# Optimization experiments

Measured on AMD Instinct MI355X. Metric: run time of the kernel, lower is better.

The kernel has to match this reference:

```python
import jax, jax.numpy as jnp
import numpy as np

DIM = 1024
HEADS = 16
HEAD_DIM = DIM // HEADS
SCALE = HEAD_DIM ** -0.5


def setup_inputs() -> dict:
    key = jax.random.key(0)
    ks = jax.random.split(key, 6)
    B, N, C = 2, 2048, DIM
    q = jax.random.normal(ks[0], (B, N, C), dtype=jnp.float32)
    k = jax.random.normal(ks[1], (B, N, C), dtype=jnp.float32)
    v = jax.random.normal(ks[2], (B, N, C), dtype=jnp.float32)
    # torch nn.Linear weights: out = x @ W.T (+ b); qkv has no bias (qkv_bias=False)
    W_qkv = jax.random.normal(ks[3], (3 * C, 3 * C), dtype=jnp.float32) * (3 * C) ** -0.5
    W_proj = jax.random.normal(ks[4], (C, C), dtype=jnp.float32) * C ** -0.5
    b_proj = jax.random.normal(ks[5], (C,), dtype=jnp.float32) * 0.02
    return {"q": q, "k": k, "v": v, "W_qkv": W_qkv, "W_proj": W_proj, "b_proj": b_proj}


def reference(q, k, v, W_qkv, W_proj, b_proj):
    B, N, C = q.shape
    # fused QKV projection on concatenated [q,k,v] -> [B,N,3C]
    qkv = jnp.concatenate([q, k, v], axis=-1) @ W_qkv.T
    qkv = qkv.reshape(B, N, 3, HEADS, HEAD_DIM).transpose(2, 0, 3, 1, 4)  # [3,B,H,N,hd]
    qh, kh, vh = qkv[0], qkv[1], qkv[2]
    attn = jnp.einsum('bhqd,bhkd->bhqk', qh, kh) * SCALE
    attn = jax.nn.softmax(attn, axis=-1)  # attn_drop is identity (p=0)
    x = jnp.einsum('bhqk,bhkd->bhqd', attn, vh)  # [B,H,N,hd]
    x = x.transpose(0, 2, 1, 3).reshape(B, N, C)
    x = x @ W_proj.T + b_proj  # proj_drop is identity (p=0)
    return x
```

## Files before the change

kernel.cpp:

```cpp
#include <hip/hip_runtime.h>
#include <hip/hip_bf16.h>
#include <stdint.h>

#define HEADS 16
#define HD 64
#define SEQ 2048
#define BATCH 2
#define CDIM 1024
#define MROWS (BATCH*SEQ)
#define K3C (3*CDIM)
#define QSCALE 0.1803368801111244f

typedef __bf16 bf16x8 __attribute__((ext_vector_type(8)));
typedef float  f32x4  __attribute__((ext_vector_type(4)));

__device__ __forceinline__ unsigned short f2bf(float f) {
    __hip_bfloat16 h = __float2bfloat16(f);
    return __builtin_bit_cast(unsigned short, h);
}
__device__ __forceinline__ unsigned int pack2bf(float a, float b) {
    return (unsigned int)f2bf(a) | ((unsigned int)f2bf(b) << 16);
}
__device__ __forceinline__ bf16x8 frag(uint4 u) { return __builtin_bit_cast(bf16x8, u); }

__device__ __forceinline__ void async16(const unsigned short* g, unsigned short* lds) {
    __builtin_amdgcn_global_load_lds(
        (const __attribute__((address_space(1))) unsigned int*)g,
        (__attribute__((address_space(3))) unsigned int*)lds, 16, 0, 0);
}

__global__ void cast_all(const float* __restrict__ q, const float* __restrict__ k,
                         const float* __restrict__ v, const float* __restrict__ Wq,
                         const float* __restrict__ Wp,
                         unsigned short* __restrict__ A, unsigned short* __restrict__ Wqb,
                         unsigned short* __restrict__ Wpb)
{
    const int bid = blockIdx.x;
    const int t = threadIdx.x;
    if (bid < MROWS) {
        const float* srcs[3] = {q, k, v};
        #pragma unroll
        for (int i = 0; i < 3; ++i) {
            float4 f = *(const float4*)(srcs[i] + (size_t)bid*CDIM + t*4);
            ushort4 s;
            s.x = f2bf(f.x); s.y = f2bf(f.y); s.z = f2bf(f.z); s.w = f2bf(f.w);
            *(ushort4*)(A + (size_t)bid*K3C + i*CDIM + t*4) = s;
        }
    } else if (bid < MROWS + 9216) {
        int idx = (bid - MROWS)*256 + t;
        float4 f = ((const float4*)Wq)[idx];
        ushort4 s;
        s.x = f2bf(f.x); s.y = f2bf(f.y); s.z = f2bf(f.z); s.w = f2bf(f.w);
        ((ushort4*)Wqb)[idx] = s;
    } else {
        int idx = (bid - MROWS - 9216)*256 + t;
        float4 f = ((const float4*)Wp)[idx];
        ushort4 s;
        s.x = f2bf(f.x); s.y = f2bf(f.y); s.z = f2bf(f.z); s.w = f2bf(f.w);
        ((ushort4*)Wpb)[idx] = s;
    }
}

template<int EPI>
__global__ __launch_bounds__(256, 2)
void gemm_bt(const unsigned short* __restrict__ A, const unsigned short* __restrict__ B,
             int M, int N, int K,
             unsigned short* __restrict__ qh, unsigned short* __restrict__ kh,
             unsigned short* __restrict__ vt,
             const float* __restrict__ bias, float* __restrict__ out)
{
    __shared__ __attribute__((aligned(16))) unsigned short As[128*32];
    __shared__ __attribute__((aligned(16))) unsigned short Bs[128*32];
    const int tid  = threadIdx.x;
    const int wave = tid >> 6;
    const int lane = tid & 63;
    const int l15  = lane & 15;
    const int quad = lane >> 4;
    const int wm = (wave >> 1) * 64;
    const int wn = (wave & 1) * 64;
    const int m0 = blockIdx.x * 128;
    const int n0 = blockIdx.y * 128;

    f32x4 acc[4][4] = {};

    const int srow = tid >> 2;
    const int sc8  = (tid & 3) * 8;

    for (int k0 = 0; k0 < K; k0 += 32) {
        #pragma unroll
        for (int t = 0; t < 2; ++t) {
            int row = t*64 + srow;
            const unsigned short* ga = A + (size_t)(m0 + row)*K + k0 + sc8;
            const unsigned short* gb = B + (size_t)(n0 + row)*K + k0 + sc8;
            async16(ga, &As[(t*256 + wave*64)*8]);
            async16(gb, &Bs[(t*256 + wave*64)*8]);
        }
        __syncthreads();
        uint4 af[4], bfv[4];
        #pragma unroll
        for (int i = 0; i < 4; ++i) {
            af[i]  = *(const uint4*)&As[(wm + i*16 + l15)*32 + quad*8];
            bfv[i] = *(const uint4*)&Bs[(wn + i*16 + l15)*32 + quad*8];
        }
        #pragma unroll
        for (int mi = 0; mi < 4; ++mi)
            #pragma unroll
            for (int ni = 0; ni < 4; ++ni)
                acc[mi][ni] = __builtin_amdgcn_mfma_f32_16x16x32_bf16(
                    frag(af[mi]), frag(bfv[ni]), acc[mi][ni], 0, 0, 0);
        __syncthreads();
    }

    if constexpr (EPI == 0) {
        #pragma unroll
        for (int mi = 0; mi < 4; ++mi) {
            int row0 = m0 + wm + mi*16 + quad*4;
            int b  = row0 >> 11;
            int nq = row0 & 2047;
            #pragma unroll
            for (int ni = 0; ni < 4; ++ni) {
                int col   = n0 + wn + ni*16 + l15;
                int which = col >> 10;
                int h     = (col >> 6) & 15;
                int d     = col & 63;
                int bh    = b*HEADS + h;
                if (which == 2) {
                    ushort4 pv;
                    pv.x = f2bf(acc[mi][ni][0]);
                    pv.y = f2bf(acc[mi][ni][1]);
                    pv.z = f2bf(acc[mi][ni][2]);
                    pv.w = f2bf(acc[mi][ni][3]);
                    *(ushort4*)&vt[((size_t)bh*HD + d)*SEQ + nq] = pv;
                } else {
                    unsigned short* dst = (which == 0) ? qh : kh;
                    float sc = (which == 0) ? QSCALE : 1.0f;
                    #pragma unroll
                    for (int r = 0; r < 4; ++r)
                        dst[((size_t)bh*SEQ + nq + r)*HD + d] = f2bf(acc[mi][ni][r] * sc);
                }
            }
        }
    } else {
        #pragma unroll
        for (int mi = 0; mi < 4; ++mi) {
            int row0 = m0 + wm + mi*16 + quad*4;
            #pragma unroll
            for (int ni = 0; ni < 4; ++ni) {
                int col  = n0 + wn + ni*16 + l15;
                float bv = bias[col];
                #pragma unroll
                for (int r = 0; r < 4; ++r)
                    out[(size_t)(row0 + r)*N + col] = acc[mi][ni][r] + bv;
            }
        }
    }
}

__global__ __launch_bounds__(256, 2)
void attention(const unsigned short* __restrict__ qh, const unsigned short* __restrict__ kh,
               const unsigned short* __restrict__ vt, unsigned short* __restrict__ xb)
{
    const int qt = blockIdx.x;
    const int h  = blockIdx.y;
    const int b  = blockIdx.z;
    const int bh = b*HEADS + h;
    const int tid  = threadIdx.x;
    const int wave = tid >> 6;
    const int lane = tid & 63;
    const int l15  = lane & 15;
    const int quad = lane >> 4;

    __shared__ __attribute__((aligned(16))) unsigned short Ks[2][64*64];
    __shared__ __attribute__((aligned(16))) unsigned short Vs[2][64*64];
    __shared__ __attribute__((aligned(16))) unsigned short Ps[4][2*16*72];

    const unsigned short* Qp = qh + ((size_t)bh*SEQ + qt*128 + wave*32)*HD;
    const unsigned short* Kp = kh + (size_t)bh*SEQ*HD;
    const unsigned short* Vp = vt + (size_t)bh*HD*SEQ;

    auto stage = [&](int kt, int bufI) {
        #pragma unroll
        for (int t = 0; t < 2; ++t) {
            int c  = t*256 + wave*64 + lane;
            int r  = c >> 3;
            int cc = (c & 7) ^ (r & 7);
            async16(Kp + (size_t)(kt*64 + r)*HD + cc*8,
                    &Ks[bufI][(t*256 + wave*64)*8]);
            async16(Vp + (size_t)r*SEQ + kt*64 + cc*8,
                    &Vs[bufI][(t*256 + wave*64)*8]);
        }
    };

    stage(0, 0);

    uint4 qf[2][2];
    #pragma unroll
    for (int g = 0; g < 2; ++g) {
        qf[g][0] = *(const uint4*)(Qp + (size_t)(g*16 + l15)*HD + quad*8);
        qf[g][1] = *(const uint4*)(Qp + (size_t)(g*16 + l15)*HD + 32 + quad*8);
    }

    f32x4 o[2][4] = {};
    float m_s[2] = {-INFINITY, -INFINITY};
    float l_s[2] = {0.f, 0.f};

    unsigned short* Pw = Ps[wave];
    const int x7 = l15 & 7;

    for (int kt = 0; kt < SEQ/64; ++kt) {
        stage((kt + 1) & 31, (kt + 1) & 1);
        asm volatile("s_waitcnt vmcnt(4)" ::: "memory");
        asm volatile("s_barrier" ::: "memory");

        const unsigned short* Kb = Ks[kt & 1];
        const unsigned short* Vb = Vs[kt & 1];

        f32x4 s[2][4];
        #pragma unroll
        for (int st = 0; st < 4; ++st) {
            int rb = st*16 + l15;
            uint4 kf0 = *(const uint4*)&Kb[(rb*8 + (quad ^ x7))*8];
            uint4 kf1 = *(const uint4*)&Kb[(rb*8 + ((4 + quad) ^ x7))*8];
            #pragma unroll
            for (int g = 0; g < 2; ++g) {
                f32x4 z = {};
                z = __builtin_amdgcn_mfma_f32_16x16x32_bf16(frag(kf0), frag(qf[g][0]), z, 0, 0, 0);
                z = __builtin_amdgcn_mfma_f32_16x16x32_bf16(frag(kf1), frag(qf[g][1]), z, 0, 0, 0);
                s[g][st] = z;
            }
        }

        #pragma unroll
        for (int g = 0; g < 2; ++g) {
            float mloc = s[g][0][0];
            #pragma unroll
            for (int st = 0; st < 4; ++st)
                #pragma unroll
                for (int r = 0; r < 4; ++r)
                    mloc = fmaxf(mloc, s[g][st][r]);
            mloc = fmaxf(mloc, __shfl_xor(mloc, 16));
            mloc = fmaxf(mloc, __shfl_xor(mloc, 32));

            float mn = fmaxf(m_s[g], mloc);
            float al = __builtin_amdgcn_exp2f(m_s[g] - mn);
            m_s[g] = mn;

            float rs = 0.f;
            float p[4][4];
            #pragma unroll
            for (int st = 0; st < 4; ++st)
                #pragma unroll
                for (int r = 0; r < 4; ++r) {
                    p[st][r] = __builtin_amdgcn_exp2f(s[g][st][r] - mn);
                    rs += p[st][r];
                }
            rs += __shfl_xor(rs, 16);
            rs += __shfl_xor(rs, 32);
            l_s[g] = al*l_s[g] + rs;

            #pragma unroll
            for (int st = 0; st < 4; ++st)
                #pragma unroll
                for (int r = 0; r < 4; ++r)
                    o[g][st][r] *= al;

            #pragma unroll
            for (int st = 0; st < 4; ++st) {
                uint2 pk;
                pk.x = pack2bf(p[st][0], p[st][1]);
                pk.y = pack2bf(p[st][2], p[st][3]);
                *(uint2*)&Pw[g*1152 + l15*72 + st*16 + quad*4] = pk;
            }
        }
        asm volatile("s_waitcnt lgkmcnt(0)" ::: "memory");

        uint4 pB[2][2];
        #pragma unroll
        for (int g = 0; g < 2; ++g) {
            pB[g][0] = *(const uint4*)&Pw[g*1152 + l15*72 + quad*8];
            pB[g][1] = *(const uint4*)&Pw[g*1152 + l15*72 + 32 + quad*8];
        }

        #pragma unroll
        for (int st = 0; st < 4; ++st) {
            int rb = st*16 + l15;
            uint4 vf0 = *(const uint4*)&Vb[(rb*8 + (quad ^ x7))*8];
            uint4 vf1 = *(const uint4*)&Vb[(rb*8 + ((4 + quad) ^ x7))*8];
            #pragma unroll
            for (int g = 0; g < 2; ++g) {
                o[g][st] = __builtin_amdgcn_mfma_f32_16x16x32_bf16(frag(vf0), frag(pB[g][0]), o[g][st], 0, 0, 0);
                o[g][st] = __builtin_amdgcn_mfma_f32_16x16x32_bf16(frag(vf1), frag(pB[g][1]), o[g][st], 0, 0, 0);
            }
        }

        asm volatile("s_barrier" ::: "memory");
    }

    #pragma unroll
    for (int g = 0; g < 2; ++g) {
        float inv = 1.0f / l_s[g];
        #pragma unroll
        for (int st = 0; st < 4; ++st) {
            uint2 pk;
            pk.x = pack2bf(o[g][st][0]*inv, o[g][st][1]*inv);
            pk.y = pack2bf(o[g][st][2]*inv, o[g][st][3]*inv);
            *(uint2*)&Pw[g*1152 + l15*72 + st*16 + quad*4] = pk;
        }
    }
    asm volatile("s_waitcnt lgkmcnt(0)" ::: "memory");

    const int qr = lane >> 2;
    const int dd = (lane & 3) * 16;
    #pragma unroll
    for (int g = 0; g < 2; ++g) {
        uint4 oa = *(const uint4*)&Pw[g*1152 + qr*72 + dd];
        uint4 ob = *(const uint4*)&Pw[g*1152 + qr*72 + dd + 8];
        const int mrow = b*SEQ + qt*128 + wave*32 + g*16 + qr;
        *(uint4*)&xb[(size_t)mrow*CDIM + h*HD + dd]     = oa;
        *(uint4*)&xb[(size_t)mrow*CDIM + h*HD + dd + 8] = ob;
    }
}

extern "C" void kernel_launch(void* const* d_in, const int* in_sizes, int n_in,
                              void* d_out, int out_size, void* d_ws, size_t ws_size,
                              hipStream_t stream)
{
    const float* q  = (const float*)d_in[0];
    const float* k  = (const float*)d_in[1];
    const float* v  = (const float*)d_in[2];
    const float* Wq = (const float*)d_in[3];
    const float* Wp = (const float*)d_in[4];
    const float* bp = (const float*)d_in[5];
    float* out = (float*)d_out;

    char* p = (char*)d_ws;
    auto carve = [&](size_t bytes) { char* r = p; p += (bytes + 255) & ~(size_t)255; return r; };
    unsigned short* Abuf   = (unsigned short*)carve((size_t)MROWS*K3C*2);
    unsigned short* Wqkvb  = (unsigned short*)carve((size_t)K3C*K3C*2);
    unsigned short* Wprojb = (unsigned short*)carve((size_t)CDIM*CDIM*2);
    unsigned short* qhb    = (unsigned short*)carve((size_t)BATCH*HEADS*SEQ*HD*2);
    unsigned short* khb    = (unsigned short*)carve((size_t)BATCH*HEADS*SEQ*HD*2);
    unsigned short* vtb    = (unsigned short*)carve((size_t)BATCH*HEADS*SEQ*HD*2);
    unsigned short* xbuf   = (unsigned short*)carve((size_t)MROWS*CDIM*2);

    cast_all<<<MROWS + 9216 + 1024, 256, 0, stream>>>(q, k, v, Wq, Wp, Abuf, Wqkvb, Wprojb);

    gemm_bt<0><<<dim3(MROWS/128, K3C/128), 256, 0, stream>>>(
        Abuf, Wqkvb, MROWS, K3C, K3C, qhb, khb, vtb, nullptr, nullptr);

    attention<<<dim3(SEQ/128, HEADS, BATCH), 256, 0, stream>>>(qhb, khb, vtb, xbuf);

    gemm_bt<1><<<dim3(MROWS/128, CDIM/128), 256, 0, stream>>>(
        xbuf, Wprojb, MROWS, CDIM, CDIM, nullptr, nullptr, nullptr, bp, out);
}
```

Baseline: 302.2 us.

## Pre-shuffle weights into MFMA fragment layout and double-buffer A tiles

The weight cast kernel now writes W into a fragment-ordered layout, so each wave can load its B operands straight from global memory into registers. This removes B from LDS, and the next k-step's B is prefetched into registers. A tiles are double-buffered in LDS using async loads, with manual waitcnt/barrier so the next tile's loads overlap the current MFMAs. This costs more registers and adds a hand-counted vmcnt that must match the number of outstanding loads.

```diff
diff --git a/kernel.cpp b/kernel.cpp
--- a/kernel.cpp
+++ b/kernel.cpp
@@ -29,6 +29,24 @@
         (__attribute__((address_space(3))) unsigned int*)lds, 16, 0, 0);
 }
 
+__device__ __forceinline__ void shuf_cell(const float* __restrict__ W, unsigned short* __restrict__ Ws,
+                                          int N, int K, int bid, int t)
+{
+    const int KG = K >> 7;
+    const int nt = bid / KG;
+    const int kc = (bid % KG)*4 + (t >> 6);
+    const int idx = t & 63;
+    const int l15 = idx & 15;
+    const int quad = idx >> 4;
+    const float* src = W + (size_t)(nt*16 + l15)*K + kc*32 + quad*8;
+    float4 f0 = *(const float4*)(src);
+    float4 f1 = *(const float4*)(src + 4);
+    uint4 d;
+    d.x = pack2bf(f0.x, f0.y); d.y = pack2bf(f0.z, f0.w);
+    d.z = pack2bf(f1.x, f1.y); d.w = pack2bf(f1.z, f1.w);
+    *(uint4*)(Ws + ((size_t)nt*(K>>5) + kc)*512 + l15*32 + quad*8) = d;
+}
+
 __global__ void cast_all(const float* __restrict__ q, const float* __restrict__ k,
                          const float* __restrict__ v, const float* __restrict__ Wq,
                          const float* __restrict__ Wp,
@@ -46,31 +64,22 @@
             s.x = f2bf(f.x); s.y = f2bf(f.y); s.z = f2bf(f.z); s.w = f2bf(f.w);
             *(ushort4*)(A + (size_t)bid*K3C + i*CDIM + t*4) = s;
         }
-    } else if (bid < MROWS + 9216) {
-        int idx = (bid - MROWS)*256 + t;
-        float4 f = ((const float4*)Wq)[idx];
-        ushort4 s;
-        s.x = f2bf(f.x); s.y = f2bf(f.y); s.z = f2bf(f.z); s.w = f2bf(f.w);
-        ((ushort4*)Wqb)[idx] = s;
+    } else if (bid < MROWS + 4608) {
+        shuf_cell(Wq, Wqb, K3C, K3C, bid - MROWS, t);
     } else {
-        int idx = (bid - MROWS - 9216)*256 + t;
-        float4 f = ((const float4*)Wp)[idx];
-        ushort4 s;
-        s.x = f2bf(f.x); s.y = f2bf(f.y); s.z = f2bf(f.z); s.w = f2bf(f.w);
-        ((ushort4*)Wpb)[idx] = s;
+        shuf_cell(Wp, Wpb, CDIM, CDIM, bid - MROWS - 4608, t);
     }
 }
 
 template<int EPI>
 __global__ __launch_bounds__(256, 2)
-void gemm_bt(const unsigned short* __restrict__ A, const unsigned short* __restrict__ B,
-             int M, int N, int K,
-             unsigned short* __restrict__ qh, unsigned short* __restrict__ kh,
-             unsigned short* __restrict__ vt,
-             const float* __restrict__ bias, float* __restrict__ out)
-{
-    __shared__ __attribute__((aligned(16))) unsigned short As[128*32];
-    __shared__ __attribute__((aligned(16))) unsigned short Bs[128*32];
+void gemm_flat(const unsigned short* __restrict__ A, const unsigned short* __restrict__ Bsh,
+               int M, int N, int K,
+               unsigned short* __restrict__ qh, unsigned short* __restrict__ kh,
+               unsigned short* __restrict__ vt,
+               const float* __restrict__ bias, float* __restrict__ out)
+{
+    __shared__ __attribute__((aligned(16))) unsigned short As[2][128*32];
     const int tid  = threadIdx.x;
     const int wave = tid >> 6;
     const int lane = tid & 63;
@@ -80,35 +89,61 @@
     const int wn = (wave & 1) * 64;
     const int m0 = blockIdx.x * 128;
     const int n0 = blockIdx.y * 128;
+    const int KC = K >> 5;
 
     f32x4 acc[4][4] = {};
 
     const int srow = tid >> 2;
     const int sc8  = (tid & 3) * 8;
 
-    for (int k0 = 0; k0 < K; k0 += 32) {
+    auto stageA = [&](int kc, int bufI) {
         #pragma unroll
         for (int t = 0; t < 2; ++t) {
             int row = t*64 + srow;
-            const unsigned short* ga = A + (size_t)(m0 + row)*K + k0 + sc8;
-            const unsigned short* gb = B + (size_t)(n0 + row)*K + k0 + sc8;
-            async16(ga, &As[(t*256 + wave*64)*8]);
-            async16(gb, &Bs[(t*256 + wave*64)*8]);
-        }
-        __syncthreads();
-        uint4 af[4], bfv[4];
-        #pragma unroll
-        for (int i = 0; i < 4; ++i) {
-            af[i]  = *(const uint4*)&As[(wm + i*16 + l15)*32 + quad*8];
-            bfv[i] = *(const uint4*)&Bs[(wn + i*16 + l15)*32 + quad*8];
-        }
+            async16(A + (size_t)(m0 + row)*K + kc*32 + sc8,
+                    &As[bufI][(t*256 + wave*64)*8]);
+        }
+    };
+
+    const unsigned short* bbase = Bsh + ((size_t)((n0 + wn) >> 4) * KC) * 512 + l15*32 + quad*8;
+
+    uint4 bcur[4], bnxt[4];
+    #pragma unroll
+    for (int i = 0; i < 4; ++i)
+        bcur[i] = *(const uint4*)(bbase + (size_t)i*KC*512);
+    stageA(0, 0);
+
+    #pragma unroll 2
+    for (int kc = 0; kc < KC; ++kc) {
+        int kn = kc + 1;
+        if (kn < KC) {
+            #pragma unroll
+            for (int i = 0; i < 4; ++i)
+                bnxt[i] = *(const uint4*)(bbase + (size_t)i*KC*512 + (size_t)kn*512);
+            stageA(kn, kn & 1);
+            asm volatile("s_waitcnt vmcnt(6)" ::: "memory");
+        } else {
+            asm volatile("s_waitcnt vmcnt(0)" ::: "memory");
+        }
+        asm volatile("s_barrier" ::: "memory");
+
+        const unsigned short* Ab = As[kc & 1];
+        uint4 af[4];
+        #pragma unroll
+        for (int i = 0; i < 4; ++i)
+            af[i] = *(const uint4*)&Ab[(wm + i*16 + l15)*32 + quad*8];
+
         #pragma unroll
         for (int mi = 0; mi < 4; ++mi)
             #pragma unroll
             for (int ni = 0; ni < 4; ++ni)
                 acc[mi][ni] = __builtin_amdgcn_mfma_f32_16x16x32_bf16(
-                    frag(af[mi]), frag(bfv[ni]), acc[mi][ni], 0, 0, 0);
-        __syncthreads();
+                    frag(af[mi]), frag(bcur[ni]), acc[mi][ni], 0, 0, 0);
+
+        #pragma unroll
+        for (int i = 0; i < 4; ++i) bcur[i] = bnxt[i];
+
+        asm volatile("s_barrier" ::: "memory");
     }
 
     if constexpr (EPI == 0) {
@@ -343,13 +378,13 @@
     unsigned short* vtb    = (unsigned short*)carve((size_t)BATCH*HEADS*SEQ*HD*2);
     unsigned short* xbuf   = (unsigned short*)carve((size_t)MROWS*CDIM*2);
 
-    cast_all<<<MROWS + 9216 + 1024, 256, 0, stream>>>(q, k, v, Wq, Wp, Abuf, Wqkvb, Wprojb);
-
-    gemm_bt<0><<<dim3(MROWS/128, K3C/128), 256, 0, stream>>>(
+    cast_all<<<MROWS + 4608 + 512, 256, 0, stream>>>(q, k, v, Wq, Wp, Abuf, Wqkvb, Wprojb);
+
+    gemm_flat<0><<<dim3(MROWS/128, K3C/128), 256, 0, stream>>>(
         Abuf, Wqkvb, MROWS, K3C, K3C, qhb, khb, vtb, nullptr, nullptr);
 
     attention<<<dim3(SEQ/128, HEADS, BATCH), 256, 0, stream>>>(qhb, khb, vtb, xbuf);
 
-    gemm_bt<1><<<dim3(MROWS/128, CDIM/128), 256, 0, stream>>>(
+    gemm_flat<1><<<dim3(MROWS/128, CDIM/128), 256, 0, stream>>>(
         xbuf, Wprojb, MROWS, CDIM, CDIM, nullptr, nullptr, nullptr, bp, out);
 }
```

After: 315.6 us. 1.04x slower.
